# Optimization experiments

Hardware: AMD Instinct MI355X
Metric: run time of the kernel (lower is better)

Reference implementation:

```python
import jax, jax.numpy as jnp
import numpy as np

# Mesh / batch constants (see shape_source)
V, E, B = 150000, 900000, 2
N, BE = B * V, B * E


def _ln(x, axes):
    # LayerNorm without affine params (per-edge normalization)
    mu = jnp.mean(x, axis=axes, keepdims=True)
    var = jnp.var(x, axis=axes, keepdims=True)
    return (x - mu) * jax.lax.rsqrt(var + 1e-5)


def setup_inputs() -> dict:
    key = jax.random.key(0)
    ks = jax.random.split(key, 10)
    x = jax.random.normal(ks[0], (N, 3), dtype=jnp.float32)
    edge_index = jax.random.randint(ks[1], (2, BE), 0, N)
    edge_attrs = jax.random.normal(ks[2], (E, 20), dtype=jnp.float32)
    # orthonormal-ish frames are fine as random for a numerics baseline
    H2frame = jax.random.normal(ks[3], (E, 2, 3), dtype=jnp.float32)
    HyperPT = jax.random.normal(ks[4], (E, 2, 2), dtype=jnp.float32)
    option_mask = jax.random.randint(ks[5], (E,), 0, 3) - 1  # values in {-1,0,1}
    broadcastmap = jax.random.randint(ks[6], (V,), 0, V)     # vertex -> tree root
    k = jnp.ones((V, 3, 3), dtype=jnp.float32)
    k2 = jnp.ones((V, 3, 3), dtype=jnp.float32)
    attn_p = jnp.ones((V, 2, 3), dtype=jnp.float32)
    att = jax.random.normal(ks[7], (1, 6), dtype=jnp.float32) * 0.1
    W1 = jax.random.normal(ks[8], (1, 2), dtype=jnp.float32)
    b1 = jnp.zeros((1,), dtype=jnp.float32)
    c = jnp.ones((2,), dtype=jnp.float32)
    return {"x": x, "edge_index": edge_index, "edge_attrs": edge_attrs,
            "H2frame": H2frame, "HyperPT": HyperPT, "option_mask": option_mask,
            "broadcastmap": broadcastmap, "k": k, "k2": k2, "attn_p": attn_p,
            "att": att, "W1": W1, "b1": b1, "c": c}


def _forward(x, edge_attrs, H2frame, HyperPT, k, k2, attn_p, att, W1, b1, c,
             edge_index, option_mask, broadcastmap):
    src, dst = edge_index[0], edge_index[1]

    def tile(a):  # repeat edge data batch_size times along dim 0
        return jnp.tile(a, (B,) + (1,) * (a.ndim - 1))

    Theta = tile(edge_attrs[:, 9:10])                 # [BE,1]
    e1 = tile(edge_attrs[:, 11:14])                   # [BE,3]
    e2 = tile(edge_attrs[:, 14:17])
    e3 = tile(edge_attrs[:, 17:20])
    cos, sin = jnp.cos(Theta), jnp.sin(Theta)
    xdir, ydir = tile(H2frame[:, 0]), tile(H2frame[:, 1])  # [BE,3]
    T = tile(HyperPT)                                  # [BE,2,2]
    om = jnp.tile(option_mask, B)                      # [BE]

    x_j = x[src]                                       # gather source feats [BE,3]
    x_i = x[dst]

    # --- parallel_transport_unmasked ---
    a = jnp.sum(e1 * x_j, -1, keepdims=True)
    b = jnp.sum(e2 * x_j, -1, keepdims=True)
    pt1 = a * cos * e1 + a * sin * e3 + b * e2         # spherical-option transport
    a2 = jnp.sum(xdir * x_j, -1, keepdims=True)
    b2 = jnp.sum(ydir * x_j, -1, keepdims=True)
    local = jnp.concatenate([a2, b2], -1)              # [BE,2]
    lc2 = jnp.einsum('eij,ej->ei', T, local)           # hyperbolic-option transport
    pt2 = xdir * lc2[:, 0:1] + ydir * lc2[:, 1:2]
    pt = (pt1 * (om == 1)[:, None] + pt2 * (om == -1)[:, None]
          + x_j * (om == 0)[:, None])                  # [BE,3]

    # --- tree-broadcast curvature gather: vertex -> root -> curvature tensors ---
    roots = broadcastmap[dst % V]                      # [BE]
    k_e, k2_e, a_e = k[roots], k2[roots], attn_p[roots]
    m1 = jnp.einsum('eij,ej->ei', k_e, pt)             # [BE,3]
    m2 = jnp.einsum('eij,ej->ei', k2_e, pt)
    feats = _ln(jnp.stack([m1, m2], -1), (1, 2))       # layernormA: [BE,3,2]
    s = _ln(jnp.einsum('ecd,edc->ec', a_e, feats), (1,))  # layernormB: [BE,2]

    # --- attention scores + segment softmax over destination nodes ---
    gat = jax.nn.leaky_relu(jnp.concatenate([x_i, pt], -1) @ att[0], 0.2)  # [BE]
    lin = (s @ W1.T + b1)[:, 0]                        # linear1: [BE]
    score = gat + lin
    smax = jax.ops.segment_max(score, dst, num_segments=N)
    exps = jnp.exp(score - smax[dst])
    denom = jax.ops.segment_sum(exps, dst, num_segments=N)
    alpha = exps / (denom[dst] + 1e-16)                # [BE]

    msg = alpha[:, None] * (pt + c[0] * m1 + c[1] * m2)  # [BE,3]
    return jax.ops.segment_sum(msg, dst, num_segments=N)  # aggr='add' -> [N,3]


def reference(x, edge_index, edge_attrs, H2frame, HyperPT, option_mask,
              broadcastmap, k, k2, attn_p, att, W1, b1, c):
    return _forward(x, edge_attrs, H2frame, HyperPT, k, k2, attn_p, att, W1, b1, c,
                    edge_index, option_mask, broadcastmap)
```

## Files before the change

kernel.cpp:

```cpp
#include <hip/hip_runtime.h>
#include <math.h>

#define VV 150000
#define EE 900000
#define NN 300000
#define BEG 1800000

struct EO { float ex, v0, v1, v2; };

__device__ __forceinline__ EO edge_math(
    float ptx, float pty, float ptz,
    const float* K1, const float* K2, const float* A,
    float xi0, float xi1, float xi2,
    float at0, float at1, float at2, float at3, float at4, float at5,
    float w0, float w1, float bb, float c0, float c1)
{
    float m10 = K1[0]*ptx + K1[1]*pty + K1[2]*ptz;
    float m11 = K1[3]*ptx + K1[4]*pty + K1[5]*ptz;
    float m12 = K1[6]*ptx + K1[7]*pty + K1[8]*ptz;
    float m20 = K2[0]*ptx + K2[1]*pty + K2[2]*ptz;
    float m21 = K2[3]*ptx + K2[4]*pty + K2[5]*ptz;
    float m22 = K2[6]*ptx + K2[7]*pty + K2[8]*ptz;
    float mu = (m10+m11+m12+m20+m21+m22)*(1.0f/6.0f);
    float d0=m10-mu, d1=m11-mu, d2=m12-mu, d3=m20-mu, d4=m21-mu, d5=m22-mu;
    float var=(d0*d0+d1*d1+d2*d2+d3*d3+d4*d4+d5*d5)*(1.0f/6.0f);
    float rA=rsqrtf(var+1e-5f);
    float s0=(A[0]*d0+A[1]*d1+A[2]*d2)*rA;
    float s1=(A[3]*d3+A[4]*d4+A[5]*d5)*rA;
    float mu2=0.5f*(s0+s1);
    float f0=s0-mu2, f1=s1-mu2;
    float var2=0.5f*(f0*f0+f1*f1);
    float rB=rsqrtf(var2+1e-5f);
    float g = xi0*at0+xi1*at1+xi2*at2+ptx*at3+pty*at4+ptz*at5;
    float gat = (g>0.0f)? g : 0.2f*g;
    float score = gat + (f0*rB)*w0 + (f1*rB)*w1 + bb;
    float ex = expf(score);
    EO o;
    o.ex = ex;
    o.v0 = ex*(ptx + c0*m10 + c1*m20);
    o.v1 = ex*(pty + c0*m11 + c1*m21);
    o.v2 = ex*(ptz + c0*m12 + c1*m22);
    return o;
}

__device__ __forceinline__ void load_kka(
    int root, const float* __restrict__ kk, const float* __restrict__ kk2,
    const float* __restrict__ ap, float* K1, float* K2, float* A)
{
    const float* p1 = kk  + (size_t)root*9;
    const float* p2 = kk2 + (size_t)root*9;
    const float* pa = ap  + (size_t)root*6;
#pragma unroll
    for (int i=0;i<9;i++) K1[i]=p1[i];
#pragma unroll
    for (int i=0;i<9;i++) K2[i]=p2[i];
#pragma unroll
    for (int i=0;i<6;i++) A[i]=pa[i];
}

__global__ __launch_bounds__(256) void k_padx(const float* __restrict__ x,
                                              float* __restrict__ xp)
{
    int v = blockIdx.x * blockDim.x + threadIdx.x;
    if (v >= NN) return;
    float4 o = {x[3*v+0], x[3*v+1], x[3*v+2], 0.0f};
    reinterpret_cast<float4*>(xp)[v] = o;
}

__global__ __launch_bounds__(256) void k_reformat(
    const float* __restrict__ kk, const float* __restrict__ kk2,
    const float* __restrict__ ap, float* __restrict__ pr)
{
    int r = blockIdx.x * blockDim.x + threadIdx.x;
    if (r >= VV) return;
    const float* p1 = kk  + (size_t)r * 9;
    const float* p2 = kk2 + (size_t)r * 9;
    const float* pa = ap  + (size_t)r * 6;
    float4* o = reinterpret_cast<float4*>(pr + (size_t)r * 24);
    float4 q0 = {p1[0], p1[1], p1[2], p1[3]};
    float4 q1 = {p1[4], p1[5], p1[6], p1[7]};
    float4 q2 = {p1[8], p2[0], p2[1], p2[2]};
    float4 q3 = {p2[3], p2[4], p2[5], p2[6]};
    float4 q4 = {p2[7], p2[8], pa[0], pa[1]};
    float4 q5 = {pa[2], pa[3], pa[4], pa[5]};
    o[0]=q0; o[1]=q1; o[2]=q2; o[3]=q3; o[4]=q4; o[5]=q5;
}

__global__ __launch_bounds__(256) void k_edge_pt(
    const float* __restrict__ xp, const int* __restrict__ ei,
    const float* __restrict__ ea, const float* __restrict__ h2,
    const float* __restrict__ hp, const int* __restrict__ omask,
    const int* __restrict__ bmap, const float* __restrict__ kk,
    const float* __restrict__ kk2, const float* __restrict__ ap,
    const float* __restrict__ att, const float* __restrict__ W1,
    const float* __restrict__ b1, const float* __restrict__ cc,
    int* __restrict__ count, float4* __restrict__ payload,
    float* __restrict__ spill, int MD)
{
    int e = blockIdx.x * blockDim.x + threadIdx.x;
    if (e >= BEG) return;

    int src = ei[e];
    int dst = ei[BEG + e];
    int eix = (e >= EE) ? (e - EE) : e;

    const float4* row = reinterpret_cast<const float4*>(ea + (size_t)eix * 20 + 8);
    float4 r0 = row[0];
    float4 r1 = row[1];
    float4 r2 = row[2];
    float Theta = r0.y;
    float e1x = r0.w, e1y = r1.x, e1z = r1.y;
    float e2x = r1.z, e2y = r1.w, e2z = r2.x;
    float e3x = r2.y, e3y = r2.z, e3z = r2.w;
    float snv, cs;
    sincosf(Theta, &snv, &cs);

    float4 xj = reinterpret_cast<const float4*>(xp)[src];

    float a = e1x*xj.x + e1y*xj.y + e1z*xj.z;
    float b = e2x*xj.x + e2y*xj.y + e2z*xj.z;
    float acs = a*cs, asn = a*snv;
    float pt1x = acs*e1x + asn*e3x + b*e2x;
    float pt1y = acs*e1y + asn*e3y + b*e2y;
    float pt1z = acs*e1z + asn*e3z + b*e2z;

    const float2* h2p = reinterpret_cast<const float2*>(h2 + (size_t)eix * 6);
    float2 h0 = h2p[0], h1 = h2p[1], h2v = h2p[2];
    float xdx = h0.x, xdy = h0.y, xdz = h1.x;
    float ydx = h1.y, ydy = h2v.x, ydz = h2v.y;
    float a2 = xdx*xj.x + xdy*xj.y + xdz*xj.z;
    float b2 = ydx*xj.x + ydy*xj.y + ydz*xj.z;
    float4 T = *reinterpret_cast<const float4*>(hp + (size_t)eix * 4);
    float l0 = T.x*a2 + T.y*b2;
    float l1 = T.z*a2 + T.w*b2;
    float pt2x = xdx*l0 + ydx*l1;
    float pt2y = xdy*l0 + ydy*l1;
    float pt2z = xdz*l0 + ydz*l1;

    int om = omask[eix];
    float ptx = (om == 1) ? pt1x : ((om == -1) ? pt2x : xj.x);
    float pty = (om == 1) ? pt1y : ((om == -1) ? pt2y : xj.y);
    float ptz = (om == 1) ? pt1z : ((om == -1) ? pt2z : xj.z);

    int slot = atomicAdd(count + dst, 1);
    if (slot < MD) {
        float4 pl = {ptx, pty, ptz, 0.0f};
        payload[(size_t)dst * MD + slot] = pl;
    } else {
        int dm = (dst >= VV) ? dst - VV : dst;
        int root = bmap[dm];
        float K1[9], K2[9], A[6];
        load_kka(root, kk, kk2, ap, K1, K2, A);
        float4 xi = reinterpret_cast<const float4*>(xp)[dst];
        EO o = edge_math(ptx, pty, ptz, K1, K2, A, xi.x, xi.y, xi.z,
                         att[0], att[1], att[2], att[3], att[4], att[5],
                         W1[0], W1[1], b1[0], cc[0], cc[1]);
        atomicAdd(spill + 4*(size_t)dst + 0, o.v0);
        atomicAdd(spill + 4*(size_t)dst + 1, o.v1);
        atomicAdd(spill + 4*(size_t)dst + 2, o.v2);
        atomicAdd(spill + 4*(size_t)dst + 3, o.ex);
    }
}

__global__ __launch_bounds__(256) void k_gather(
    const float* __restrict__ xp, const int* __restrict__ bmap,
    const float* __restrict__ pr,
    const float* __restrict__ att, const float* __restrict__ W1,
    const float* __restrict__ b1, const float* __restrict__ cc,
    const int* __restrict__ count, const float4* __restrict__ payload,
    const float4* __restrict__ spill, float* __restrict__ out, int MD)
{
    int v = blockIdx.x * blockDim.x + threadIdx.x;
    if (v >= NN) return;
    int dm = (v >= VV) ? v - VV : v;
    int root = bmap[dm];
    const float4* P = reinterpret_cast<const float4*>(pr + (size_t)root * 24);
    float4 p0 = P[0], p1 = P[1], p2 = P[2], p3 = P[3], p4 = P[4], p5 = P[5];
    float K1[9] = {p0.x,p0.y,p0.z,p0.w,p1.x,p1.y,p1.z,p1.w,p2.x};
    float K2[9] = {p2.y,p2.z,p2.w,p3.x,p3.y,p3.z,p3.w,p4.x,p4.y};
    float A[6]  = {p4.z,p4.w,p5.x,p5.y,p5.z,p5.w};

    float4 xi = reinterpret_cast<const float4*>(xp)[v];
    float at0=att[0], at1=att[1], at2=att[2], at3=att[3], at4=att[4], at5=att[5];
    float w0=W1[0], w1=W1[1], bb=b1[0], c0=cc[0], c1=cc[1];

    int deg = count[v];
    int lim = deg < MD ? deg : MD;
    float n0=0.f, n1=0.f, n2=0.f, dn=0.f;
    for (int i = 0; i < lim; ++i) {
        float4 p = payload[(size_t)v * MD + i];
        EO o = edge_math(p.x, p.y, p.z, K1, K2, A, xi.x, xi.y, xi.z,
                         at0, at1, at2, at3, at4, at5, w0, w1, bb, c0, c1);
        n0 += o.v0; n1 += o.v1; n2 += o.v2; dn += o.ex;
    }
    float4 sp = spill[v];
    n0 += sp.x; n1 += sp.y; n2 += sp.z; dn += sp.w;

    float inv = 1.0f / (dn + 1e-16f);
    out[3*v+0] = n0 * inv;
    out[3*v+1] = n1 * inv;
    out[3*v+2] = n2 * inv;
}

extern "C" void kernel_launch(void* const* d_in, const int* in_sizes, int n_in,
                              void* d_out, int out_size, void* d_ws, size_t ws_size,
                              hipStream_t stream) {
    const float* x    = (const float*)d_in[0];
    const int*   ei   = (const int*)d_in[1];
    const float* ea   = (const float*)d_in[2];
    const float* h2   = (const float*)d_in[3];
    const float* hp   = (const float*)d_in[4];
    const int*   om   = (const int*)d_in[5];
    const int*   bmap = (const int*)d_in[6];
    const float* kk   = (const float*)d_in[7];
    const float* kk2  = (const float*)d_in[8];
    const float* ap   = (const float*)d_in[9];
    const float* att  = (const float*)d_in[10];
    const float* W1   = (const float*)d_in[11];
    const float* b1   = (const float*)d_in[12];
    const float* cc   = (const float*)d_in[13];
    float* out = (float*)d_out;

    float* ws = (float*)d_ws;
    int*    count   = (int*)ws;
    float*  spill   = ws + (size_t)NN;
    float*  xp      = ws + (size_t)5 * NN;
    float*  pr      = ws + (size_t)9 * NN;
    float4* payload = (float4*)(pr + (size_t)VV * 24);

    size_t fixed = (size_t)NN * 36 + (size_t)VV * 96;
    int MD = 16;
    if (ws_size < fixed + (size_t)NN * 16 * 16) MD = 12;
    if (ws_size < fixed + (size_t)NN * 16 * 12) MD = 8;

    hipMemsetAsync(ws, 0, (size_t)NN * 20, stream);

    const int blk = 256;
    k_padx<<<(NN + blk - 1) / blk, blk, 0, stream>>>(x, xp);
    k_reformat<<<(VV + blk - 1) / blk, blk, 0, stream>>>(kk, kk2, ap, pr);
    k_edge_pt<<<(BEG + blk - 1) / blk, blk, 0, stream>>>(
        xp, ei, ea, h2, hp, om, bmap, kk, kk2, ap, att, W1, b1, cc,
        count, payload, spill, MD);
    k_gather<<<(NN + blk - 1) / blk, blk, 0, stream>>>(
        xp, bmap, pr, att, W1, b1, cc,
        count, payload, (const float4*)spill, out, MD);
}
```

Measured before the change: 322.1 us.

## Parallelize gather over edges per node with 16-lane shuffle reduction

The gather kernel now assigns 16 threads to each destination node instead of one. Each lane processes one payload slot and recomputes the edge math, and the lanes combine their partial sums with xor shuffles within a 16-wide group. This removes the serial per-node loop and its divergence across nodes with different degrees. In exchange it launches 16x more threads, and every active lane reloads the per-root parameters and x. Lanes past the node's degree sit idle, and with an average degree of about 6 that is roughly two thirds of them.

```diff
diff --git a/kernel.cpp b/kernel.cpp
--- a/kernel.cpp
+++ b/kernel.cpp
@@ -162,7 +162,7 @@
     }
 }
 
-__global__ __launch_bounds__(256) void k_gather(
+__global__ __launch_bounds__(256) void k_gather2(
     const float* __restrict__ xp, const int* __restrict__ bmap,
     const float* __restrict__ pr,
     const float* __restrict__ att, const float* __restrict__ W1,
@@ -170,36 +170,47 @@
     const int* __restrict__ count, const float4* __restrict__ payload,
     const float4* __restrict__ spill, float* __restrict__ out, int MD)
 {
-    int v = blockIdx.x * blockDim.x + threadIdx.x;
+    int g = blockIdx.x * blockDim.x + threadIdx.x;
+    int v = g >> 4;
+    int i = g & 15;
     if (v >= NN) return;
-    int dm = (v >= VV) ? v - VV : v;
-    int root = bmap[dm];
-    const float4* P = reinterpret_cast<const float4*>(pr + (size_t)root * 24);
-    float4 p0 = P[0], p1 = P[1], p2 = P[2], p3 = P[3], p4 = P[4], p5 = P[5];
-    float K1[9] = {p0.x,p0.y,p0.z,p0.w,p1.x,p1.y,p1.z,p1.w,p2.x};
-    float K2[9] = {p2.y,p2.z,p2.w,p3.x,p3.y,p3.z,p3.w,p4.x,p4.y};
-    float A[6]  = {p4.z,p4.w,p5.x,p5.y,p5.z,p5.w};
-
-    float4 xi = reinterpret_cast<const float4*>(xp)[v];
-    float at0=att[0], at1=att[1], at2=att[2], at3=att[3], at4=att[4], at5=att[5];
-    float w0=W1[0], w1=W1[1], bb=b1[0], c0=cc[0], c1=cc[1];
 
     int deg = count[v];
     int lim = deg < MD ? deg : MD;
-    float n0=0.f, n1=0.f, n2=0.f, dn=0.f;
-    for (int i = 0; i < lim; ++i) {
+
+    EO o; o.ex = 0.f; o.v0 = 0.f; o.v1 = 0.f; o.v2 = 0.f;
+    if (i < lim) {
         float4 p = payload[(size_t)v * MD + i];
-        EO o = edge_math(p.x, p.y, p.z, K1, K2, A, xi.x, xi.y, xi.z,
-                         at0, at1, at2, at3, at4, at5, w0, w1, bb, c0, c1);
-        n0 += o.v0; n1 += o.v1; n2 += o.v2; dn += o.ex;
-    }
-    float4 sp = spill[v];
-    n0 += sp.x; n1 += sp.y; n2 += sp.z; dn += sp.w;
-
-    float inv = 1.0f / (dn + 1e-16f);
-    out[3*v+0] = n0 * inv;
-    out[3*v+1] = n1 * inv;
-    out[3*v+2] = n2 * inv;
+        int dm = (v >= VV) ? v - VV : v;
+        int root = bmap[dm];
+        const float4* P = reinterpret_cast<const float4*>(pr + (size_t)root * 24);
+        float4 p0 = P[0], p1 = P[1], p2 = P[2], p3 = P[3], p4 = P[4], p5 = P[5];
+        float K1[9] = {p0.x,p0.y,p0.z,p0.w,p1.x,p1.y,p1.z,p1.w,p2.x};
+        float K2[9] = {p2.y,p2.z,p2.w,p3.x,p3.y,p3.z,p3.w,p4.x,p4.y};
+        float A[6]  = {p4.z,p4.w,p5.x,p5.y,p5.z,p5.w};
+        float4 xi = reinterpret_cast<const float4*>(xp)[v];
+        o = edge_math(p.x, p.y, p.z, K1, K2, A, xi.x, xi.y, xi.z,
+                      att[0], att[1], att[2], att[3], att[4], att[5],
+                      W1[0], W1[1], b1[0], cc[0], cc[1]);
+    }
+
+#pragma unroll
+    for (int off = 8; off > 0; off >>= 1) {
+        o.ex += __shfl_xor(o.ex, off, 16);
+        o.v0 += __shfl_xor(o.v0, off, 16);
+        o.v1 += __shfl_xor(o.v1, off, 16);
+        o.v2 += __shfl_xor(o.v2, off, 16);
+    }
+
+    if (i == 0) {
+        float4 sp = spill[v];
+        float n0 = o.v0 + sp.x, n1 = o.v1 + sp.y, n2 = o.v2 + sp.z;
+        float dn = o.ex + sp.w;
+        float inv = 1.0f / (dn + 1e-16f);
+        out[3*v+0] = n0 * inv;
+        out[3*v+1] = n1 * inv;
+        out[3*v+2] = n2 * inv;
+    }
 }
 
 extern "C" void kernel_launch(void* const* d_in, const int* in_sizes, int n_in,
@@ -241,7 +252,7 @@
     k_edge_pt<<<(BEG + blk - 1) / blk, blk, 0, stream>>>(
         xp, ei, ea, h2, hp, om, bmap, kk, kk2, ap, att, W1, b1, cc,
         count, payload, spill, MD);
-    k_gather<<<(NN + blk - 1) / blk, blk, 0, stream>>>(
+    k_gather2<<<((size_t)NN * 16 + blk - 1) / blk, blk, 0, stream>>>(
         xp, bmap, pr, att, W1, b1, cc,
         count, payload, (const float4*)spill, out, MD);
 }
```

Measured after the change: 320.9 us. Within noise of the previous version (-0.4%).
